# Kernel optimization log

Hardware: AMD Instinct MI355X
Metric: run time of the kernel (lower is better)

## Reference

```python
import jax, jax.numpy as jnp
import numpy as np

HIDDEN_DIM = 2048
CODE_DIM = 256
CODEBOOK_SIZE = 512
FC_DIMS = [1024, 512]
BATCH = 16384
EPS = 1e-5
NEG_SLOPE = 0.01  # PyTorch LeakyReLU default


def _linear_init(key, fan_in, fan_out):
    # kaiming_uniform_(a=sqrt(3)) ~= U(-1/sqrt(fan_in), 1/sqrt(fan_in)) scaled; use uniform bound
    bound = 1.0 / np.sqrt(fan_in)
    return jax.random.uniform(key, (fan_in, fan_out), jnp.float32, -bound, bound)


def setup_inputs() -> dict:
    key = jax.random.key(0)
    ks = jax.random.split(key, 16)
    h = jax.random.normal(ks[0], (BATCH, HIDDEN_DIM), jnp.float32)
    # encoder: Linear(2048->1024, no bias), BN, LReLU, Linear(1024->512, no bias), BN, LReLU, Linear(512->256, bias)
    enc_w1 = _linear_init(ks[1], HIDDEN_DIM, FC_DIMS[0])
    enc_bn1_g = jnp.ones((FC_DIMS[0],), jnp.float32)
    enc_bn1_b = jnp.zeros((FC_DIMS[0],), jnp.float32)
    enc_w2 = _linear_init(ks[2], FC_DIMS[0], FC_DIMS[1])
    enc_bn2_g = jnp.ones((FC_DIMS[1],), jnp.float32)
    enc_bn2_b = jnp.zeros((FC_DIMS[1],), jnp.float32)
    enc_w3 = _linear_init(ks[3], FC_DIMS[1], CODE_DIM)
    enc_b3 = jax.random.uniform(ks[4], (CODE_DIM,), jnp.float32, -1/np.sqrt(FC_DIMS[1]), 1/np.sqrt(FC_DIMS[1]))
    # codebook: NearestEmbed weight shape (code_dim, codebook_size)
    codebook = jax.random.normal(ks[5], (CODE_DIM, CODEBOOK_SIZE), jnp.float32)
    # decoder: Linear(256->512, no bias), BN, LReLU, Linear(512->1024, no bias), BN, LReLU, Linear(1024->2048, bias)
    dec_w1 = _linear_init(ks[6], CODE_DIM, FC_DIMS[1])
    dec_bn1_g = jnp.ones((FC_DIMS[1],), jnp.float32)
    dec_bn1_b = jnp.zeros((FC_DIMS[1],), jnp.float32)
    dec_w2 = _linear_init(ks[7], FC_DIMS[1], FC_DIMS[0])
    dec_bn2_g = jnp.ones((FC_DIMS[0],), jnp.float32)
    dec_bn2_b = jnp.zeros((FC_DIMS[0],), jnp.float32)
    dec_w3 = _linear_init(ks[8], FC_DIMS[0], HIDDEN_DIM)
    dec_b3 = jax.random.uniform(ks[9], (HIDDEN_DIM,), jnp.float32, -1/np.sqrt(FC_DIMS[0]), 1/np.sqrt(FC_DIMS[0]))
    return dict(h=h, enc_w1=enc_w1, enc_bn1_g=enc_bn1_g, enc_bn1_b=enc_bn1_b,
                enc_w2=enc_w2, enc_bn2_g=enc_bn2_g, enc_bn2_b=enc_bn2_b,
                enc_w3=enc_w3, enc_b3=enc_b3, codebook=codebook,
                dec_w1=dec_w1, dec_bn1_g=dec_bn1_g, dec_bn1_b=dec_bn1_b,
                dec_w2=dec_w2, dec_bn2_g=dec_bn2_g, dec_bn2_b=dec_bn2_b,
                dec_w3=dec_w3, dec_b3=dec_b3)


def _bn(x, g, b):
    # BatchNorm1d, training mode: biased batch variance, eps=1e-5
    mu = jnp.mean(x, axis=0)
    var = jnp.var(x, axis=0)
    return (x - mu) * jax.lax.rsqrt(var + EPS) * g + b


def _lrelu(x):
    return jnp.where(x >= 0, x, NEG_SLOPE * x)


def _quantize(z_e, codebook):
    # nearest codebook entry; codebook is [code_dim, K]
    # dist[b,k] = ||z_e[b] - codebook[:,k]||^2 (expanded, drop constant ||z||^2 for argmin? keep full for clarity)
    d = (jnp.sum(z_e * z_e, axis=1, keepdims=True)
         - 2.0 * (z_e @ codebook)
         + jnp.sum(codebook * codebook, axis=0)[None, :])  # [B, K]
    idx = jnp.argmin(d, axis=1)  # [B]
    z_q = codebook.T[idx]        # [B, code_dim]
    return z_q, idx


def reference(h, enc_w1, enc_bn1_g, enc_bn1_b, enc_w2, enc_bn2_g, enc_bn2_b,
              enc_w3, enc_b3, codebook,
              dec_w1, dec_bn1_g, dec_bn1_b, dec_w2, dec_bn2_g, dec_bn2_b,
              dec_w3, dec_b3):
    # encoder
    x = _lrelu(_bn(h @ enc_w1, enc_bn1_g, enc_bn1_b))
    x = _lrelu(_bn(x @ enc_w2, enc_bn2_g, enc_bn2_b))
    z_e = x @ enc_w3 + enc_b3  # [B, code_dim]
    # nearest-embed quantization with straight-through estimator
    z_q_raw, code_indices = _quantize(z_e, codebook)
    z_q = z_e + jax.lax.stop_gradient(z_q_raw - z_e)
    # decoder
    y = _lrelu(_bn(z_q @ dec_w1, dec_bn1_g, dec_bn1_b))
    y = _lrelu(_bn(y @ dec_w2, dec_bn2_g, dec_bn2_b))
    h_recon = y @ dec_w3 + dec_b3  # [B, hidden_dim]
    return z_e, z_q, h_recon, code_indices
```

## Files before the change

### kernel.cpp

```cpp
#include <hip/hip_runtime.h>
#include <hip/hip_fp16.h>
#include <cstdint>
#include <cstddef>

typedef _Float16 f16;
typedef _Float16 half8 __attribute__((ext_vector_type(8)));
typedef _Float16 half4 __attribute__((ext_vector_type(4)));
typedef float floatx4 __attribute__((ext_vector_type(4)));

static constexpr size_t NB  = 16384;
static constexpr size_t DH  = 2048;
static constexpr size_t F1  = 1024;
static constexpr size_t F2  = 512;
static constexpr size_t CD  = 256;
static constexpr size_t KCB = 512;

static constexpr size_t ZE_OFF  = 0;
static constexpr size_t ZQ_OFF  = NB * CD;
static constexpr size_t HR_OFF  = 2 * NB * CD;
static constexpr size_t IDX_OFF = 2 * NB * CD + NB * DH;

static constexpr size_t O_HH   = 0;
static constexpr size_t O_HL   = O_HH + NB * DH * 2;
static constexpr size_t R1_END = O_HL + NB * DH * 2;

static constexpr size_t R_X1H = 0;
static constexpr size_t R_X1L = NB * F1 * 2;
static constexpr size_t R_X2F = 2 * NB * F1 * 2;
static constexpr size_t R_X2H = R_X2F + NB * F2 * 4;
static constexpr size_t R_X2L = R_X2H + NB * F2 * 2;
static constexpr size_t R_Y1F = 0;
static constexpr size_t R_Y1H = NB * F2 * 4;
static constexpr size_t R_Y2H = 0;

static constexpr size_t O_W1H = R1_END;
static constexpr size_t O_W1L = O_W1H + F1 * DH * 2;
static constexpr size_t O_W2H = O_W1L + F1 * DH * 2;
static constexpr size_t O_W2L = O_W2H + F2 * F1 * 2;
static constexpr size_t O_W3H = O_W2L + F2 * F1 * 2;
static constexpr size_t O_W3L = O_W3H + CD * F2 * 2;
static constexpr size_t O_CBH = O_W3L + CD * F2 * 2;
static constexpr size_t O_CBL = O_CBH + KCB * CD * 2;
static constexpr size_t O_DW1 = O_CBL + KCB * CD * 2;
static constexpr size_t O_DW2 = O_DW1 + F2 * CD * 2;
static constexpr size_t O_DW3 = O_DW2 + F1 * F2 * 2;
static constexpr size_t O_SUM = O_DW3 + DH * F1 * 2;
static constexpr size_t O_SQ  = O_SUM + 4 * 1024 * 8;
static constexpr size_t O_CN  = O_SQ + 4 * 1024 * 8;
static constexpr size_t R2    = (O_CN + 4096 + 255) & ~(size_t)255;
static constexpr size_t R2_X1F = R2;
static constexpr size_t R2_ZEH = R2;
static constexpr size_t R2_ZEL = R2 + NB * CD * 2;
static constexpr size_t R2_S   = R2 + 2 * NB * CD * 2;
static constexpr size_t R2_ZQH = R2_S + NB * KCB * 4;
static constexpr size_t R2_Y2F = R2;

#define GLLDS(src, dst)                                                          \
    __builtin_amdgcn_global_load_lds(                                            \
        (const __attribute__((address_space(1))) void*)(src),                    \
        (__attribute__((address_space(3))) void*)(dst), 16, 0, 0)

#define VMCNT(n)  asm volatile("s_waitcnt vmcnt(" #n ")" ::: "memory")

#define WAITC(n) do { switch (n) {                                               \
    case 0: asm volatile("s_waitcnt lgkmcnt(0)" ::: "memory"); break;            \
    case 1: asm volatile("s_waitcnt lgkmcnt(1)" ::: "memory"); break;            \
    case 2: asm volatile("s_waitcnt lgkmcnt(2)" ::: "memory"); break;            \
    case 3: asm volatile("s_waitcnt lgkmcnt(3)" ::: "memory"); break;            \
    case 4: asm volatile("s_waitcnt lgkmcnt(4)" ::: "memory"); break;            \
    case 5: asm volatile("s_waitcnt lgkmcnt(5)" ::: "memory"); break;            \
    case 6: asm volatile("s_waitcnt lgkmcnt(6)" ::: "memory"); break;            \
    default: asm volatile("s_waitcnt lgkmcnt(7)" ::: "memory"); break; }         \
    __builtin_amdgcn_sched_barrier(0); } while (0)

template<int MW, bool BIAS, bool STATS, bool WSPLIT>
__global__ __launch_bounds__(512)
void gemm3_t(const f16* __restrict__ Ah_, const f16* __restrict__ Al_,
             const f16* __restrict__ Bh_, const f16* __restrict__ Bl_,
             float* __restrict__ C, const float* __restrict__ bias,
             double* __restrict__ ssum, double* __restrict__ ssq,
             f16* __restrict__ zeh, f16* __restrict__ zel,
             int M, int N, int K)
{
    constexpr int BM = MW * 32;
    __shared__ f16 lds[2][2][16384];
    const int tid  = threadIdx.x;
    const int lane = tid & 63;
    const int w    = tid >> 6;
    const int wr   = w >> 2, wn = w & 3;
    const int row0 = blockIdx.x * BM;
    const int col0 = blockIdx.y * 256;

    const int rr8 = lane >> 3;
    const int p   = (lane & 7) ^ rr8;
    const int rr  = w * 32 + rr8;
    const int arr = rr & (BM - 1);
    const f16* srcH = (p < 4) ? (Ah_ + (size_t)(row0 + arr) * K + p * 8)
                              : (Bh_ + (size_t)(col0 + rr) * K + (p - 4) * 8);
    const f16* srcL = (p < 4) ? (Al_ + (size_t)(row0 + arr) * K + p * 8)
                              : (Bl_ + (size_t)(col0 + rr) * K + (p - 4) * 8);
    const int dstBase = w * 32 * 64;
    const int KT = K >> 5;

    floatx4 acc[MW][4];
#pragma unroll
    for (int m = 0; m < MW; ++m)
#pragma unroll
        for (int n = 0; n < 4; ++n)
#pragma unroll
            for (int j = 0; j < 4; ++j) acc[m][n][j] = 0.f;

    const int l15 = lane & 15;
    const int sA  = lane >> 4;

    int rdA[MW], rdB[4];
#pragma unroll
    for (int m = 0; m < MW; ++m) {
        const int rA = wr * (MW * 16) + m * 16 + l15;
        rdA[m] = rA * 64 + ((sA ^ (rA & 7)) << 3);
    }
#pragma unroll
    for (int n = 0; n < 4; ++n) {
        const int rB = wn * 64 + n * 16 + l15;
        rdB[n] = rB * 64 + (((4 + sA) ^ (rB & 7)) << 3);
    }

#pragma unroll
    for (int j = 0; j < 4; ++j)
        GLLDS(srcH + (size_t)j * 8 * K, &lds[0][0][dstBase + j * 512]);
#pragma unroll
    for (int j = 0; j < 4; ++j)
        GLLDS(srcL + (size_t)j * 8 * K, &lds[0][1][dstBase + j * 512]);
    VMCNT(4);
    __builtin_amdgcn_s_barrier();

    half8 afh[MW], afl[MW], bfh[4], bfl[4];

    for (int kt = 0; kt < KT; ++kt) {
        const int cur = kt & 1, nxt = cur ^ 1;
        const int koff = (kt + 1 < KT ? kt + 1 : kt) << 5;
        const f16* plH = lds[cur][0];
        const f16* plL = lds[cur][1];

#pragma unroll
        for (int n = 0; n < 4; ++n) bfh[n] = *(const half8*)(plH + rdB[n]);
        afh[0] = *(const half8*)(plH + rdA[0]);
        afh[1] = *(const half8*)(plH + rdA[1]);
#pragma unroll
        for (int j = 0; j < 4; ++j)
            GLLDS(srcH + (size_t)j * 8 * K + koff, &lds[nxt][0][dstBase + j * 512]);
        WAITC(1);
        __builtin_amdgcn_s_setprio(1);
#pragma unroll
        for (int m = 0; m < MW; ++m) {
            if (m + 2 < MW) afh[m + 2] = *(const half8*)(plH + rdA[m + 2]);
#pragma unroll
            for (int n = 0; n < 4; ++n)
                acc[m][n] = __builtin_amdgcn_mfma_f32_16x16x32_f16(afh[m], bfh[n], acc[m][n], 0, 0, 0);
            if (m + 1 < MW) { if (m + 2 < MW) WAITC(1); else WAITC(0); }
        }
        __builtin_amdgcn_s_setprio(0);
        VMCNT(4);
        __builtin_amdgcn_s_barrier();

#pragma unroll
        for (int n = 0; n < 4; ++n) bfl[n] = *(const half8*)(plL + rdB[n]);
        afl[0] = *(const half8*)(plL + rdA[0]);
        afl[1] = *(const half8*)(plL + rdA[1]);
#pragma unroll
        for (int j = 0; j < 4; ++j)
            GLLDS(srcL + (size_t)j * 8 * K + koff, &lds[nxt][1][dstBase + j * 512]);
        WAITC(2);
        __builtin_amdgcn_s_setprio(1);
#pragma unroll
        for (int m = 0; m < MW; ++m) {
            if (m + 2 < MW) afl[m + 2] = *(const half8*)(plL + rdA[m + 2]);
#pragma unroll
            for (int n = 0; n < 4; ++n)
                acc[m][n] = __builtin_amdgcn_mfma_f32_16x16x32_f16(afh[m], bfl[n], acc[m][n], 0, 0, 0);
        }
#pragma unroll
        for (int m = 0; m < MW; ++m) {
            WAITC(MW - 1 - m);
#pragma unroll
            for (int n = 0; n < 4; ++n)
                acc[m][n] = __builtin_amdgcn_mfma_f32_16x16x32_f16(afl[m], bfh[n], acc[m][n], 0, 0, 0);
        }
        __builtin_amdgcn_s_setprio(0);
        VMCNT(4);
        __builtin_amdgcn_s_barrier();
    }
    VMCNT(0);

    const int cb0 = col0 + wn * 64;
    const int rb0 = row0 + wr * (MW * 16) + (lane >> 4) * 4;
#pragma unroll
    for (int n = 0; n < 4; ++n) {
        const int col = cb0 + n * 16 + l15;
        const float bv = BIAS ? bias[col] : 0.f;
        double sd = 0.0, sq = 0.0;
#pragma unroll
        for (int m = 0; m < MW; ++m) {
            const int row = rb0 + m * 16;
#pragma unroll
            for (int j = 0; j < 4; ++j) {
                const float v = acc[m][n][j] + bv;
                const size_t o = (size_t)(row + j) * N + col;
                C[o] = v;
                if (WSPLIT) {
                    const f16 hv = (f16)v;
                    zeh[o] = hv;
                    zel[o] = (f16)(v - (float)hv);
                }
                if (STATS) { sd += (double)v; sq += (double)v * (double)v; }
            }
        }
        if (STATS) {
            sd += __shfl_xor(sd, 16);
            sd += __shfl_xor(sd, 32);
            sq += __shfl_xor(sq, 16);
            sq += __shfl_xor(sq, 32);
            if (lane < 16) {
                atomicAdd(ssum + col, sd);
                atomicAdd(ssq + col, sq);
            }
        }
    }
}

template<int MW, bool BIAS, bool STATS>
__global__ __launch_bounds__(512)
void gemm1_t(const f16* __restrict__ A_, const f16* __restrict__ B_,
             float* __restrict__ C, const float* __restrict__ bias,
             double* __restrict__ ssum, double* __restrict__ ssq,
             int M, int N, int K)
{
    constexpr int BM = MW * 32;
    __shared__ f16 lds[3][16384];
    const int tid  = threadIdx.x;
    const int lane = tid & 63;
    const int w    = tid >> 6;
    const int wr   = w >> 2, wn = w & 3;
    const int row0 = blockIdx.x * BM;
    const int col0 = blockIdx.y * 256;

    const int rr8 = lane >> 3;
    const int p   = (lane & 7) ^ rr8;
    const int rr  = w * 32 + rr8;
    const int arr = rr & (BM - 1);
    const f16* srcH = (p < 4) ? (A_ + (size_t)(row0 + arr) * K + p * 8)
                              : (B_ + (size_t)(col0 + rr) * K + (p - 4) * 8);
    const int dstBase = w * 32 * 64;
    const int KT = K >> 5;

    floatx4 acc[MW][4];
#pragma unroll
    for (int m = 0; m < MW; ++m)
#pragma unroll
        for (int n = 0; n < 4; ++n)
#pragma unroll
            for (int j = 0; j < 4; ++j) acc[m][n][j] = 0.f;

    const int l15 = lane & 15;
    const int sA  = lane >> 4;

    int rdA[MW], rdB[4];
#pragma unroll
    for (int m = 0; m < MW; ++m) {
        const int rA = wr * (MW * 16) + m * 16 + l15;
        rdA[m] = rA * 64 + ((sA ^ (rA & 7)) << 3);
    }
#pragma unroll
    for (int n = 0; n < 4; ++n) {
        const int rB = wn * 64 + n * 16 + l15;
        rdB[n] = rB * 64 + (((4 + sA) ^ (rB & 7)) << 3);
    }

#pragma unroll
    for (int j = 0; j < 4; ++j)
        GLLDS(srcH + (size_t)j * 8 * K, &lds[0][dstBase + j * 512]);
    {
        const int k1 = (KT > 1 ? 1 : 0) << 5;
#pragma unroll
        for (int j = 0; j < 4; ++j)
            GLLDS(srcH + (size_t)j * 8 * K + k1, &lds[1][dstBase + j * 512]);
    }
    VMCNT(4);
    __builtin_amdgcn_s_barrier();

    half8 afh[MW], bfh[4];

    for (int kt = 0; kt < KT; ++kt) {
        const int cur = kt % 3, tgt = (kt + 2) % 3;
        const int koff = (kt + 2 < KT ? kt + 2 : KT - 1) << 5;
        const f16* plH = lds[cur];

#pragma unroll
        for (int n = 0; n < 4; ++n) bfh[n] = *(const half8*)(plH + rdB[n]);
        afh[0] = *(const half8*)(plH + rdA[0]);
        afh[1] = *(const half8*)(plH + rdA[1]);
#pragma unroll
        for (int j = 0; j < 4; ++j)
            GLLDS(srcH + (size_t)j * 8 * K + koff, &lds[tgt][dstBase + j * 512]);
        WAITC(1);
        __builtin_amdgcn_s_setprio(1);
#pragma unroll
        for (int m = 0; m < MW; ++m) {
            if (m + 2 < MW) afh[m + 2] = *(const half8*)(plH + rdA[m + 2]);
#pragma unroll
            for (int n = 0; n < 4; ++n)
                acc[m][n] = __builtin_amdgcn_mfma_f32_16x16x32_f16(afh[m], bfh[n], acc[m][n], 0, 0, 0);
            if (m + 1 < MW) { if (m + 2 < MW) WAITC(1); else WAITC(0); }
        }
        __builtin_amdgcn_s_setprio(0);
        VMCNT(4);
        __builtin_amdgcn_s_barrier();
    }
    VMCNT(0);

    const int cb0 = col0 + wn * 64;
    const int rb0 = row0 + wr * (MW * 16) + (lane >> 4) * 4;
#pragma unroll
    for (int n = 0; n < 4; ++n) {
        const int col = cb0 + n * 16 + l15;
        const float bv = BIAS ? bias[col] : 0.f;
        double sd = 0.0, sq = 0.0;
#pragma unroll
        for (int m = 0; m < MW; ++m) {
            const int row = rb0 + m * 16;
#pragma unroll
            for (int j = 0; j < 4; ++j) {
                const float v = acc[m][n][j] + bv;
                C[(size_t)(row + j) * N + col] = v;
                if (STATS) { sd += (double)v; sq += (double)v * (double)v; }
            }
        }
        if (STATS) {
            sd += __shfl_xor(sd, 16);
            sd += __shfl_xor(sd, 32);
            sq += __shfl_xor(sq, 16);
            sq += __shfl_xor(sq, 32);
            if (lane < 16) {
                atomicAdd(ssum + col, sd);
                atomicAdd(ssq + col, sq);
            }
        }
    }
}

template<bool SPLIT>
__global__ void bn_applyF(const float* __restrict__ X,
                          const double* __restrict__ ssum, const double* __restrict__ ssq,
                          const float* __restrict__ g, const float* __restrict__ b,
                          f16* __restrict__ Yhi, f16* __restrict__ Ylo,
                          size_t n4, int Nmask)
{
    const size_t stride = (size_t)gridDim.x * blockDim.x;
    for (size_t i = (size_t)blockIdx.x * blockDim.x + threadIdx.x; i < n4; i += stride) {
        const floatx4 x = ((const floatx4*)X)[i];
        const int col = (int)((i * 4) & (size_t)Nmask);
        half4 hh, ll;
#pragma unroll
        for (int j = 0; j < 4; ++j) {
            const double mean = ssum[col + j] * (1.0 / (double)NB);
            const double var  = ssq[col + j] * (1.0 / (double)NB) - mean * mean;
            const double sc   = (double)g[col + j] / sqrt(var + 1e-5);
            const float scale = (float)sc;
            const float shift = (float)((double)b[col + j] - mean * sc);
            float v = x[j] * scale + shift;
            v = v >= 0.f ? v : 0.01f * v;
            const f16 hv = (f16)v;
            hh[j] = hv;
            if (SPLIT) ll[j] = (f16)(v - (float)hv);
        }
        ((half4*)Yhi)[i] = hh;
        if (SPLIT) ((half4*)Ylo)[i] = ll;
    }
}

__device__ __forceinline__ void tr_body(const float* __restrict__ W, f16* __restrict__ Thi,
                                        f16* __restrict__ Tlo, int K, int N,
                                        int bx, int by, bool split)
{
    __shared__ float tile[32][33];
    const int x = threadIdx.x;
    const int y = threadIdx.y;
    const int nt = bx * 32;
    const int kt = by * 32;
#pragma unroll
    for (int i = 0; i < 32; i += 8)
        tile[y + i][x] = W[(size_t)(kt + y + i) * N + nt + x];
    __syncthreads();
#pragma unroll
    for (int i = 0; i < 32; i += 8) {
        const float v = tile[x][y + i];
        const size_t o = (size_t)(nt + y + i) * K + kt + x;
        const f16 hv = (f16)v;
        Thi[o] = hv;
        if (split) Tlo[o] = (f16)(v - (float)hv);
    }
}

__global__ void prep_all(const float* __restrict__ h,
                         const float* __restrict__ ew1, const float* __restrict__ ew2,
                         const float* __restrict__ ew3, const float* __restrict__ cbk,
                         const float* __restrict__ dw1, const float* __restrict__ dw2,
                         const float* __restrict__ dw3,
                         f16* __restrict__ Hh, f16* __restrict__ Hl,
                         f16* __restrict__ W1h, f16* __restrict__ W1l,
                         f16* __restrict__ W2h, f16* __restrict__ W2l,
                         f16* __restrict__ W3h, f16* __restrict__ W3l,
                         f16* __restrict__ CBh, f16* __restrict__ CBl,
                         f16* __restrict__ D1t, f16* __restrict__ D2t,
                         f16* __restrict__ D3t, float* __restrict__ cn,
                         double* __restrict__ sums)
{
    const int bidx = blockIdx.x;
    const int tid = threadIdx.y * 32 + threadIdx.x;
    if (bidx < 2048) {
        const size_t n4 = NB * DH / 4;
        const size_t stride = (size_t)2048 * 256;
        for (size_t i = (size_t)bidx * 256 + tid; i < n4; i += stride) {
            const floatx4 x = ((const floatx4*)h)[i];
            half4 hh, ll;
#pragma unroll
            for (int j = 0; j < 4; ++j) {
                const float v = x[j];
                const f16 hv = (f16)v;
                hh[j] = hv;
                ll[j] = (f16)(v - (float)hv);
            }
            ((half4*)Hh)[i] = hh;
            ((half4*)Hl)[i] = ll;
        }
        return;
    }
    const int b = bidx - 2048;
    if (b < 2048)      tr_body(ew1, W1h, W1l, DH, F1, b % 32, b / 32, true);
    else if (b < 2560) { const int c = b - 2048; tr_body(ew2, W2h, W2l, F1, F2, c % 16, c / 16, true); }
    else if (b < 2688) { const int c = b - 2560; tr_body(ew3, W3h, W3l, F2, CD, c % 8,  c / 8,  true); }
    else if (b < 2816) { const int c = b - 2688; tr_body(cbk, CBh, CBl, CD, KCB, c % 16, c / 16, true); }
    else if (b < 2944) { const int c = b - 2816; tr_body(dw1, D1t, nullptr, CD, F2, c % 16, c / 16, false); }
    else if (b < 3456) { const int c = b - 2944; tr_body(dw2, D2t, nullptr, F2, F1, c % 32, c / 32, false); }
    else if (b < 5504) { const int c = b - 3456; tr_body(dw3, D3t, nullptr, F1, DH, c % 64, c / 64, false); }
    else if (b < 5506) {
        const int k = (b - 5504) * 256 + tid;
        if (k < (int)KCB) {
            double s = 0.0;
            for (int d = 0; d < (int)CD; ++d) {
                const float v = cbk[(size_t)d * KCB + k];
                s += (double)v * v;
            }
            cn[k] = (float)s;
        }
    } else {
        const int idx = (b - 5506) * 256 + tid;
        for (int i = idx; i < 8192; i += 2048) sums[i] = 0.0;
    }
}

__global__ void argmin_gather(const float* __restrict__ S, const float* __restrict__ cn,
                              const float* __restrict__ cb, float* __restrict__ zq,
                              float* __restrict__ idx_out, f16* __restrict__ zqh)
{
    const int lane = threadIdx.x & 63;
    const int row  = blockIdx.x * 4 + (threadIdx.x >> 6);
    const float* Sr = S + (size_t)row * KCB;
    float best = 3.4e38f;
    int bi = 0;
#pragma unroll
    for (int i = 0; i < 8; ++i) {
        const int k = lane + 64 * i;
        const float d = cn[k] - 2.f * Sr[k];
        if (d < best) { best = d; bi = k; }
    }
#pragma unroll
    for (int off = 32; off > 0; off >>= 1) {
        const float ob = __shfl_xor(best, off);
        const int   oi = __shfl_xor(bi, off);
        if (ob < best || (ob == best && oi < bi)) { best = ob; bi = oi; }
    }
    if (lane == 0) idx_out[row] = (float)bi;
#pragma unroll
    for (int i = 0; i < 4; ++i) {
        const int d = lane + 64 * i;
        const float v = cb[(size_t)d * KCB + bi];
        zq[(size_t)row * CD + d]  = v;
        zqh[(size_t)row * CD + d] = (f16)v;
    }
}

extern "C" void kernel_launch(void* const* d_in, const int* in_sizes, int n_in,
                              void* d_out, int out_size, void* d_ws, size_t ws_size,
                              hipStream_t stream)
{
    (void)in_sizes; (void)n_in; (void)out_size; (void)ws_size;
    const float* h   = (const float*)d_in[0];
    const float* ew1 = (const float*)d_in[1];
    const float* bg1 = (const float*)d_in[2];
    const float* bb1 = (const float*)d_in[3];
    const float* ew2 = (const float*)d_in[4];
    const float* bg2 = (const float*)d_in[5];
    const float* bb2 = (const float*)d_in[6];
    const float* ew3 = (const float*)d_in[7];
    const float* eb3 = (const float*)d_in[8];
    const float* cb  = (const float*)d_in[9];
    const float* dw1 = (const float*)d_in[10];
    const float* dg1 = (const float*)d_in[11];
    const float* db1 = (const float*)d_in[12];
    const float* dw2 = (const float*)d_in[13];
    const float* dg2 = (const float*)d_in[14];
    const float* db2 = (const float*)d_in[15];
    const float* dw3 = (const float*)d_in[16];
    const float* db3 = (const float*)d_in[17];

    char* ws = (char*)d_ws;
    float* out = (float*)d_out;

    f16* Hh  = (f16*)(ws + O_HH);
    f16* Hl  = (f16*)(ws + O_HL);
    f16* W1h = (f16*)(ws + O_W1H);
    f16* W1l = (f16*)(ws + O_W1L);
    f16* W2h = (f16*)(ws + O_W2H);
    f16* W2l = (f16*)(ws + O_W2L);
    f16* W3h = (f16*)(ws + O_W3H);
    f16* W3l = (f16*)(ws + O_W3L);
    f16* CBh = (f16*)(ws + O_CBH);
    f16* CBl = (f16*)(ws + O_CBL);
    f16* D1t = (f16*)(ws + O_DW1);
    f16* D2t = (f16*)(ws + O_DW2);
    f16* D3t = (f16*)(ws + O_DW3);
    double* sum0 = (double*)(ws + O_SUM);
    double* sq0  = (double*)(ws + O_SQ);
    float* cn  = (float*)(ws + O_CN);

    float* X1f = (float*)(ws + R2_X1F);
    f16*  X1h = (f16*)(ws + R_X1H);
    f16*  X1l = (f16*)(ws + R_X1L);
    float* X2f = (float*)(ws + R_X2F);
    f16*  X2h = (f16*)(ws + R_X2H);
    f16*  X2l = (f16*)(ws + R_X2L);
    f16*  Zeh = (f16*)(ws + R2_ZEH);
    f16*  Zel = (f16*)(ws + R2_ZEL);
    float* Sb  = (float*)(ws + R2_S);
    f16*  Zqh = (f16*)(ws + R2_ZQH);
    float* Y1f = (float*)(ws + R_Y1F);
    f16*  Y1h = (f16*)(ws + R_Y1H);
    float* Y2f = (float*)(ws + R2_Y2F);
    f16*  Y2h = (f16*)(ws + R_Y2H);

    prep_all<<<7556 + 8, dim3(32, 8), 0, stream>>>(h, ew1, ew2, ew3, cb, dw1, dw2, dw3,
        Hh, Hl, W1h, W1l, W2h, W2l, W3h, W3l, CBh, CBl, D1t, D2t, D3t, cn, sum0);

    gemm3_t<8, false, true, false><<<dim3(NB / 256, F1 / 256), 512, 0, stream>>>(
        Hh, Hl, W1h, W1l, X1f, nullptr, sum0, sq0, nullptr, nullptr, NB, F1, DH);
    bn_applyF<true><<<2048, 256, 0, stream>>>(X1f, sum0, sq0, bg1, bb1, X1h, X1l, NB * F1 / 4, (int)F1 - 1);

    gemm3_t<4, false, true, false><<<dim3(NB / 128, F2 / 256), 512, 0, stream>>>(
        X1h, X1l, W2h, W2l, X2f, nullptr, sum0 + 1024, sq0 + 1024, nullptr, nullptr, NB, F2, F1);
    bn_applyF<true><<<2048, 256, 0, stream>>>(X2f, sum0 + 1024, sq0 + 1024, bg2, bb2, X2h, X2l, NB * F2 / 4, (int)F2 - 1);

    gemm3_t<4, true, false, true><<<dim3(NB / 128, CD / 256), 512, 0, stream>>>(
        X2h, X2l, W3h, W3l, out + ZE_OFF, eb3, nullptr, nullptr, Zeh, Zel, NB, CD, F2);

    gemm3_t<4, false, false, false><<<dim3(NB / 128, KCB / 256), 512, 0, stream>>>(
        Zeh, Zel, CBh, CBl, Sb, nullptr, nullptr, nullptr, nullptr, nullptr, NB, KCB, CD);
    argmin_gather<<<NB / 4, 256, 0, stream>>>(Sb, cn, cb, out + ZQ_OFF, out + IDX_OFF, Zqh);

    gemm1_t<4, false, true><<<dim3(NB / 128, F2 / 256), 512, 0, stream>>>(
        Zqh, D1t, Y1f, nullptr, sum0 + 2048, sq0 + 2048, NB, F2, CD);
    bn_applyF<false><<<2048, 256, 0, stream>>>(Y1f, sum0 + 2048, sq0 + 2048, dg1, db1, Y1h, nullptr, NB * F2 / 4, (int)F2 - 1);

    gemm1_t<8, false, true><<<dim3(NB / 256, F1 / 256), 512, 0, stream>>>(
        Y1h, D2t, Y2f, nullptr, sum0 + 3072, sq0 + 3072, NB, F1, F2);
    bn_applyF<false><<<2048, 256, 0, stream>>>(Y2f, sum0 + 3072, sq0 + 3072, dg2, db2, Y2h, nullptr, NB * F1 / 4, (int)F1 - 1);

    gemm1_t<8, true, false><<<dim3(NB / 256, DH / 256), 512, 0, stream>>>(
        Y2h, D3t, out + HR_OFF, db3, nullptr, nullptr, NB, DH, F1);
}
```

Measured before the change: 612.4 us.

## Fuse batch-norm and LeakyReLU into GEMM epilogues via a grid-wide barrier

```diff
diff --git a/kernel.cpp b/kernel.cpp
--- a/kernel.cpp
+++ b/kernel.cpp
@@ -26,12 +26,10 @@
 
 static constexpr size_t R_X1H = 0;
 static constexpr size_t R_X1L = NB * F1 * 2;
-static constexpr size_t R_X2F = 2 * NB * F1 * 2;
-static constexpr size_t R_X2H = R_X2F + NB * F2 * 4;
+static constexpr size_t R_X2H = 2 * NB * F1 * 2;
 static constexpr size_t R_X2L = R_X2H + NB * F2 * 2;
-static constexpr size_t R_Y1F = 0;
-static constexpr size_t R_Y1H = NB * F2 * 4;
-static constexpr size_t R_Y2H = 0;
+static constexpr size_t R_Y1H = 0;
+static constexpr size_t R_Y2H = NB * F2 * 2;
 
 static constexpr size_t O_W1H = R1_END;
 static constexpr size_t O_W1L = O_W1H + F1 * DH * 2;
@@ -47,13 +45,12 @@
 static constexpr size_t O_SUM = O_DW3 + DH * F1 * 2;
 static constexpr size_t O_SQ  = O_SUM + 4 * 1024 * 8;
 static constexpr size_t O_CN  = O_SQ + 4 * 1024 * 8;
+static constexpr size_t O_CTR = O_CN + 2048;
 static constexpr size_t R2    = (O_CN + 4096 + 255) & ~(size_t)255;
-static constexpr size_t R2_X1F = R2;
 static constexpr size_t R2_ZEH = R2;
 static constexpr size_t R2_ZEL = R2 + NB * CD * 2;
 static constexpr size_t R2_S   = R2 + 2 * NB * CD * 2;
 static constexpr size_t R2_ZQH = R2_S + NB * KCB * 4;
-static constexpr size_t R2_Y2F = R2;
 
 #define GLLDS(src, dst)                                                          \
     __builtin_amdgcn_global_load_lds(                                            \
@@ -73,12 +70,24 @@
     default: asm volatile("s_waitcnt lgkmcnt(7)" ::: "memory"); break; }         \
     __builtin_amdgcn_sched_barrier(0); } while (0)
 
-template<int MW, bool BIAS, bool STATS, bool WSPLIT>
+__device__ __forceinline__ void grid_barrier(int* ctr, int nblk, int tid)
+{
+    __syncthreads();
+    if (tid == 0) {
+        atomicAdd(ctr, 1);
+        while (atomicAdd(ctr, 0) < nblk) __builtin_amdgcn_s_sleep(2);
+    }
+    __syncthreads();
+}
+
+template<int MW, bool BIAS, bool WSPLIT, bool BNFUSE>
 __global__ __launch_bounds__(512)
 void gemm3_t(const f16* __restrict__ Ah_, const f16* __restrict__ Al_,
              const f16* __restrict__ Bh_, const f16* __restrict__ Bl_,
              float* __restrict__ C, const float* __restrict__ bias,
              double* __restrict__ ssum, double* __restrict__ ssq,
+             const float* __restrict__ g, const float* __restrict__ b,
+             int* __restrict__ ctr,
              f16* __restrict__ zeh, f16* __restrict__ zel,
              int M, int N, int K)
 {
@@ -194,45 +203,77 @@
 
     const int cb0 = col0 + wn * 64;
     const int rb0 = row0 + wr * (MW * 16) + (lane >> 4) * 4;
-#pragma unroll
-    for (int n = 0; n < 4; ++n) {
-        const int col = cb0 + n * 16 + l15;
-        const float bv = BIAS ? bias[col] : 0.f;
-        double sd = 0.0, sq = 0.0;
-#pragma unroll
-        for (int m = 0; m < MW; ++m) {
-            const int row = rb0 + m * 16;
-#pragma unroll
-            for (int j = 0; j < 4; ++j) {
-                const float v = acc[m][n][j] + bv;
-                const size_t o = (size_t)(row + j) * N + col;
-                C[o] = v;
-                if (WSPLIT) {
+
+    if constexpr (BNFUSE) {
+#pragma unroll
+        for (int n = 0; n < 4; ++n) {
+            const int col = cb0 + n * 16 + l15;
+            double sd = 0.0, sq = 0.0;
+#pragma unroll
+            for (int m = 0; m < MW; ++m)
+#pragma unroll
+                for (int j = 0; j < 4; ++j) {
+                    const double v = (double)acc[m][n][j];
+                    sd += v; sq += v * v;
+                }
+            sd += __shfl_xor(sd, 16); sd += __shfl_xor(sd, 32);
+            sq += __shfl_xor(sq, 16); sq += __shfl_xor(sq, 32);
+            if (lane < 16) { atomicAdd(ssum + col, sd); atomicAdd(ssq + col, sq); }
+        }
+        grid_barrier(ctr, gridDim.x * gridDim.y, tid);
+#pragma unroll
+        for (int n = 0; n < 4; ++n) {
+            const int col = cb0 + n * 16 + l15;
+            const double mean = atomicAdd(ssum + col, 0.0) * (1.0 / (double)NB);
+            const double var  = atomicAdd(ssq + col, 0.0) * (1.0 / (double)NB) - mean * mean;
+            const double sc   = (double)g[col] / sqrt(var + 1e-5);
+            const float scale = (float)sc;
+            const float shift = (float)((double)b[col] - mean * sc);
+#pragma unroll
+            for (int m = 0; m < MW; ++m) {
+                const int row = rb0 + m * 16;
+#pragma unroll
+                for (int j = 0; j < 4; ++j) {
+                    float v = fmaf(acc[m][n][j], scale, shift);
+                    v = v >= 0.f ? v : 0.01f * v;
                     const f16 hv = (f16)v;
+                    const size_t o = (size_t)(row + j) * N + col;
                     zeh[o] = hv;
                     zel[o] = (f16)(v - (float)hv);
                 }
-                if (STATS) { sd += (double)v; sq += (double)v * (double)v; }
             }
         }
-        if (STATS) {
-            sd += __shfl_xor(sd, 16);
-            sd += __shfl_xor(sd, 32);
-            sq += __shfl_xor(sq, 16);
-            sq += __shfl_xor(sq, 32);
-            if (lane < 16) {
-                atomicAdd(ssum + col, sd);
-                atomicAdd(ssq + col, sq);
+    } else {
+#pragma unroll
+        for (int n = 0; n < 4; ++n) {
+            const int col = cb0 + n * 16 + l15;
+            const float bv = BIAS ? bias[col] : 0.f;
+#pragma unroll
+            for (int m = 0; m < MW; ++m) {
+                const int row = rb0 + m * 16;
+#pragma unroll
+                for (int j = 0; j < 4; ++j) {
+                    const float v = acc[m][n][j] + bv;
+                    const size_t o = (size_t)(row + j) * N + col;
+                    C[o] = v;
+                    if (WSPLIT) {
+                        const f16 hv = (f16)v;
+                        zeh[o] = hv;
+                        zel[o] = (f16)(v - (float)hv);
+                    }
+                }
             }
         }
     }
 }
 
-template<int MW, bool BIAS, bool STATS>
+template<int MW, bool BIAS, bool BNFUSE>
 __global__ __launch_bounds__(512)
 void gemm1_t(const f16* __restrict__ A_, const f16* __restrict__ B_,
              float* __restrict__ C, const float* __restrict__ bias,
              double* __restrict__ ssum, double* __restrict__ ssq,
+             const float* __restrict__ g, const float* __restrict__ b,
+             int* __restrict__ ctr, f16* __restrict__ yh,
              int M, int N, int K)
 {
     constexpr int BM = MW * 32;
@@ -320,61 +361,56 @@
 
     const int cb0 = col0 + wn * 64;
     const int rb0 = row0 + wr * (MW * 16) + (lane >> 4) * 4;
-#pragma unroll
-    for (int n = 0; n < 4; ++n) {
-        const int col = cb0 + n * 16 + l15;
-        const float bv = BIAS ? bias[col] : 0.f;
-        double sd = 0.0, sq = 0.0;
-#pragma unroll
-        for (int m = 0; m < MW; ++m) {
-            const int row = rb0 + m * 16;
-#pragma unroll
-            for (int j = 0; j < 4; ++j) {
-                const float v = acc[m][n][j] + bv;
-                C[(size_t)(row + j) * N + col] = v;
-                if (STATS) { sd += (double)v; sq += (double)v * (double)v; }
+
+    if constexpr (BNFUSE) {
+#pragma unroll
+        for (int n = 0; n < 4; ++n) {
+            const int col = cb0 + n * 16 + l15;
+            double sd = 0.0, sq = 0.0;
+#pragma unroll
+            for (int m = 0; m < MW; ++m)
+#pragma unroll
+                for (int j = 0; j < 4; ++j) {
+                    const double v = (double)acc[m][n][j];
+                    sd += v; sq += v * v;
+                }
+            sd += __shfl_xor(sd, 16); sd += __shfl_xor(sd, 32);
+            sq += __shfl_xor(sq, 16); sq += __shfl_xor(sq, 32);
+            if (lane < 16) { atomicAdd(ssum + col, sd); atomicAdd(ssq + col, sq); }
+        }
+        grid_barrier(ctr, gridDim.x * gridDim.y, tid);
+#pragma unroll
+        for (int n = 0; n < 4; ++n) {
+            const int col = cb0 + n * 16 + l15;
+            const double mean = atomicAdd(ssum + col, 0.0) * (1.0 / (double)NB);
+            const double var  = atomicAdd(ssq + col, 0.0) * (1.0 / (double)NB) - mean * mean;
+            const double sc   = (double)g[col] / sqrt(var + 1e-5);
+            const float scale = (float)sc;
+            const float shift = (float)((double)b[col] - mean * sc);
+#pragma unroll
+            for (int m = 0; m < MW; ++m) {
+                const int row = rb0 + m * 16;
+#pragma unroll
+                for (int j = 0; j < 4; ++j) {
+                    float v = fmaf(acc[m][n][j], scale, shift);
+                    v = v >= 0.f ? v : 0.01f * v;
+                    yh[(size_t)(row + j) * N + col] = (f16)v;
+                }
             }
         }
-        if (STATS) {
-            sd += __shfl_xor(sd, 16);
-            sd += __shfl_xor(sd, 32);
-            sq += __shfl_xor(sq, 16);
-            sq += __shfl_xor(sq, 32);
-            if (lane < 16) {
-                atomicAdd(ssum + col, sd);
-                atomicAdd(ssq + col, sq);
+    } else {
+#pragma unroll
+        for (int n = 0; n < 4; ++n) {
+            const int col = cb0 + n * 16 + l15;
+            const float bv = BIAS ? bias[col] : 0.f;
+#pragma unroll
+            for (int m = 0; m < MW; ++m) {
+                const int row = rb0 + m * 16;
+#pragma unroll
+                for (int j = 0; j < 4; ++j)
+                    C[(size_t)(row + j) * N + col] = acc[m][n][j] + bv;
             }
         }
-    }
-}
-
-template<bool SPLIT>
-__global__ void bn_applyF(const float* __restrict__ X,
-                          const double* __restrict__ ssum, const double* __restrict__ ssq,
-                          const float* __restrict__ g, const float* __restrict__ b,
-                          f16* __restrict__ Yhi, f16* __restrict__ Ylo,
-                          size_t n4, int Nmask)
-{
-    const size_t stride = (size_t)gridDim.x * blockDim.x;
-    for (size_t i = (size_t)blockIdx.x * blockDim.x + threadIdx.x; i < n4; i += stride) {
-        const floatx4 x = ((const floatx4*)X)[i];
-        const int col = (int)((i * 4) & (size_t)Nmask);
-        half4 hh, ll;
-#pragma unroll
-        for (int j = 0; j < 4; ++j) {
-            const double mean = ssum[col + j] * (1.0 / (double)NB);
-            const double var  = ssq[col + j] * (1.0 / (double)NB) - mean * mean;
-            const double sc   = (double)g[col + j] / sqrt(var + 1e-5);
-            const float scale = (float)sc;
-            const float shift = (float)((double)b[col + j] - mean * sc);
-            float v = x[j] * scale + shift;
-            v = v >= 0.f ? v : 0.01f * v;
-            const f16 hv = (f16)v;
-            hh[j] = hv;
-            if (SPLIT) ll[j] = (f16)(v - (float)hv);
-        }
-        ((half4*)Yhi)[i] = hh;
-        if (SPLIT) ((half4*)Ylo)[i] = ll;
     }
 }
 
@@ -413,7 +449,7 @@
                          f16* __restrict__ CBh, f16* __restrict__ CBl,
                          f16* __restrict__ D1t, f16* __restrict__ D2t,
                          f16* __restrict__ D3t, float* __restrict__ cn,
-                         double* __restrict__ sums)
+                         double* __restrict__ sums, int* __restrict__ ctrs)
 {
     const int bidx = blockIdx.x;
     const int tid = threadIdx.y * 32 + threadIdx.x;
@@ -456,6 +492,7 @@
     } else {
         const int idx = (b - 5506) * 256 + tid;
         for (int i = idx; i < 8192; i += 2048) sums[i] = 0.0;
+        if (idx < 8) ctrs[idx] = 0;
     }
 }
 
@@ -533,48 +570,48 @@
     double* sum0 = (double*)(ws + O_SUM);
     double* sq0  = (double*)(ws + O_SQ);
     float* cn  = (float*)(ws + O_CN);
-
-    float* X1f = (float*)(ws + R2_X1F);
+    int* ctrs  = (int*)(ws + O_CTR);
+
     f16*  X1h = (f16*)(ws + R_X1H);
     f16*  X1l = (f16*)(ws + R_X1L);
-    float* X2f = (float*)(ws + R_X2F);
     f16*  X2h = (f16*)(ws + R_X2H);
     f16*  X2l = (f16*)(ws + R_X2L);
     f16*  Zeh = (f16*)(ws + R2_ZEH);
     f16*  Zel = (f16*)(ws + R2_ZEL);
     float* Sb  = (float*)(ws + R2_S);
     f16*  Zqh = (f16*)(ws + R2_ZQH);
-    float* Y1f = (float*)(ws + R_Y1F);
     f16*  Y1h = (f16*)(ws + R_Y1H);
-    float* Y2f = (float*)(ws + R2_Y2F);
     f16*  Y2h = (f16*)(ws + R_Y2H);
 
-    prep_all<<<7556 + 8, dim3(32, 8), 0, stream>>>(h, ew1, ew2, ew3, cb, dw1, dw2, dw3,
-        Hh, Hl, W1h, W1l, W2h, W2l, W3h, W3l, CBh, CBl, D1t, D2t, D3t, cn, sum0);
-
-    gemm3_t<8, false, true, false><<<dim3(NB / 256, F1 / 256), 512, 0, stream>>>(
-        Hh, Hl, W1h, W1l, X1f, nullptr, sum0, sq0, nullptr, nullptr, NB, F1, DH);
-    bn_applyF<true><<<2048, 256, 0, stream>>>(X1f, sum0, sq0, bg1, bb1, X1h, X1l, NB * F1 / 4, (int)F1 - 1);
-
-    gemm3_t<4, false, true, false><<<dim3(NB / 128, F2 / 256), 512, 0, stream>>>(
-        X1h, X1l, W2h, W2l, X2f, nullptr, sum0 + 1024, sq0 + 1024, nullptr, nullptr, NB, F2, F1);
-    bn_applyF<true><<<2048, 256, 0, stream>>>(X2f, sum0 + 1024, sq0 + 1024, bg2, bb2, X2h, X2l, NB * F2 / 4, (int)F2 - 1);
-
-    gemm3_t<4, true, false, true><<<dim3(NB / 128, CD / 256), 512, 0, stream>>>(
-        X2h, X2l, W3h, W3l, out + ZE_OFF, eb3, nullptr, nullptr, Zeh, Zel, NB, CD, F2);
+    prep_all<<<7564, dim3(32, 8), 0, stream>>>(h, ew1, ew2, ew3, cb, dw1, dw2, dw3,
+        Hh, Hl, W1h, W1l, W2h, W2l, W3h, W3l, CBh, CBl, D1t, D2t, D3t, cn, sum0, ctrs);
+
+    gemm3_t<8, false, false, true><<<dim3(NB / 256, F1 / 256), 512, 0, stream>>>(
+        Hh, Hl, W1h, W1l, nullptr, nullptr, sum0, sq0, bg1, bb1, ctrs + 0,
+        X1h, X1l, NB, F1, DH);
+
+    gemm3_t<4, false, false, true><<<dim3(NB / 128, F2 / 256), 512, 0, stream>>>(
+        X1h, X1l, W2h, W2l, nullptr, nullptr, sum0 + 1024, sq0 + 1024, bg2, bb2, ctrs + 1,
+        X2h, X2l, NB, F2, F1);
+
+    gemm3_t<4, true, true, false><<<dim3(NB / 128, CD / 256), 512, 0, stream>>>(
+        X2h, X2l, W3h, W3l, out + ZE_OFF, eb3, nullptr, nullptr, nullptr, nullptr, nullptr,
+        Zeh, Zel, NB, CD, F2);
 
     gemm3_t<4, false, false, false><<<dim3(NB / 128, KCB / 256), 512, 0, stream>>>(
-        Zeh, Zel, CBh, CBl, Sb, nullptr, nullptr, nullptr, nullptr, nullptr, NB, KCB, CD);
+        Zeh, Zel, CBh, CBl, Sb, nullptr, nullptr, nullptr, nullptr, nullptr, nullptr,
+        nullptr, nullptr, NB, KCB, CD);
     argmin_gather<<<NB / 4, 256, 0, stream>>>(Sb, cn, cb, out + ZQ_OFF, out + IDX_OFF, Zqh);
 
     gemm1_t<4, false, true><<<dim3(NB / 128, F2 / 256), 512, 0, stream>>>(
-        Zqh, D1t, Y1f, nullptr, sum0 + 2048, sq0 + 2048, NB, F2, CD);
-    bn_applyF<false><<<2048, 256, 0, stream>>>(Y1f, sum0 + 2048, sq0 + 2048, dg1, db1, Y1h, nullptr, NB * F2 / 4, (int)F2 - 1);
+        Zqh, D1t, nullptr, nullptr, sum0 + 2048, sq0 + 2048, dg1, db1, ctrs + 2,
+        Y1h, NB, F2, CD);
 
     gemm1_t<8, false, true><<<dim3(NB / 256, F1 / 256), 512, 0, stream>>>(
-        Y1h, D2t, Y2f, nullptr, sum0 + 3072, sq0 + 3072, NB, F1, F2);
-    bn_applyF<false><<<2048, 256, 0, stream>>>(Y2f, sum0 + 3072, sq0 + 3072, dg2, db2, Y2h, nullptr, NB * F1 / 4, (int)F1 - 1);
+        Y1h, D2t, nullptr, nullptr, sum0 + 3072, sq0 + 3072, dg2, db2, ctrs + 3,
+        Y2h, NB, F1, F2);
 
     gemm1_t<8, true, false><<<dim3(NB / 256, DH / 256), 512, 0, stream>>>(
-        Y2h, D3t, out + HR_OFF, db3, nullptr, nullptr, NB, DH, F1);
+        Y2h, D3t, out + HR_OFF, db3, nullptr, nullptr, nullptr, nullptr, nullptr,
+        nullptr, NB, DH, F1);
 }
```

After: 804.1 us. +31.3%, slower.
